# Performance work log

Measured on AMD Instinct MI355X. Metric: run time of the kernel, lower is better.

## Reference

```python
import jax, jax.numpy as jnp
import numpy as np

FACTOR = 3   # ProbAttention factor hardcoded in Informer.__init__
N_HEADS = 8


def _ln(x, g, b, eps=1e-5):
    m = x.mean(-1, keepdims=True)
    v = ((x - m) ** 2).mean(-1, keepdims=True)
    return (x - m) / jnp.sqrt(v + eps) * g + b


def _pos_emb(L, d_model):
    # standard fixed sinusoidal positional embedding (Informer PositionalEmbedding)
    pos = np.arange(L, dtype=np.float32)[:, None]
    div = np.exp(np.arange(0, d_model, 2, dtype=np.float32) * (-np.log(10000.0) / d_model))
    pe = np.zeros((L, d_model), np.float32)
    pe[:, 0::2] = np.sin(pos * div)
    pe[:, 1::2] = np.cos(pos * div)
    return jnp.asarray(pe)


def _prob_attention(q, k, v, rng_key):
    # q,k,v: [B, L, H, D]; mask_flag=False, scale=None -> 1/sqrt(D)
    B, L, H, D = q.shape
    Q = q.transpose(0, 2, 1, 3)
    K = k.transpose(0, 2, 1, 3)
    V = v.transpose(0, 2, 1, 3)
    L_Q = L_K = L
    U_part = min(FACTOR * int(np.ceil(np.log(L_K))), L_K)   # sampled keys per query
    u = min(FACTOR * int(np.ceil(np.log(L_Q))), L_Q)        # top queries kept
    # sample keys (shared across batch/heads, as in torch.randint(L_K,(L_Q,sample_k)))
    idx_sample = jax.random.randint(rng_key, (L_Q, U_part), 0, L_K)
    K_sample = K[:, :, idx_sample, :]                        # [B,H,L_Q,U_part,D]
    QK_sample = jnp.einsum('bhld,bhlsd->bhls', Q, K_sample)  # [B,H,L_Q,U_part]
    M = QK_sample.max(-1) - QK_sample.sum(-1) / L_K          # sparsity measure [B,H,L_Q]
    _, idx_top = jax.lax.top_k(M, u)                         # [B,H,u]
    Q_reduce = jnp.take_along_axis(Q, idx_top[..., None], axis=2)          # [B,H,u,D]
    scores = jnp.einsum('bhud,bhkd->bhuk', Q_reduce, K) / jnp.sqrt(jnp.float32(D))
    attn = jax.nn.softmax(scores, axis=-1)
    upd = jnp.einsum('bhuk,bhkd->bhud', attn, V)             # [B,H,u,D]
    # initial context = mean over values (mask_flag=False), overwrite at top queries
    ctx = jnp.broadcast_to(V.mean(axis=2, keepdims=True), (B, H, L_Q, D))
    bI = jnp.arange(B)[:, None, None]
    hI = jnp.arange(H)[None, :, None]
    ctx = ctx.at[bI, hI, idx_top].set(upd)
    return ctx.transpose(0, 2, 1, 3).reshape(B, L, H * D)


def _forward(x, time_features, g_in, b_in, W_tok, W_time, b_time,
             Wq, bq, Wk, bk, Wv, bv, Wo, bo, W1, b1, W2, b2,
             g1, be1, g2, be2, g_enc, b_enc, W_pre, b_pre, W_fc, b_fc):
    B, L, _ = x.shape
    d_model = W_tok.shape[-1]
    H = N_HEADS
    D = d_model // H
    x = _ln(x, g_in, b_in)                                   # input_norm over enc_in
    # DataEmbedding: circular Conv1d(k=3) token emb + positional + timeF linear
    xp = jnp.pad(x, ((0, 0), (1, 1), (0, 0)), mode='wrap')
    tok = jax.lax.conv_general_dilated(xp, W_tok, (1,), 'VALID',
                                       dimension_numbers=('NWC', 'WIO', 'NWC'))
    h = tok + _pos_emb(L, d_model)[None] + time_features @ W_time.T + b_time
    key = jax.random.key(42)
    for i in range(Wq.shape[0]):                              # e_layers (small, fixed)
        q = (h @ Wq[i].T + bq[i]).reshape(B, L, H, D)
        k = (h @ Wk[i].T + bk[i]).reshape(B, L, H, D)
        v = (h @ Wv[i].T + bv[i]).reshape(B, L, H, D)
        attn_out = _prob_attention(q, k, v, jax.random.fold_in(key, i))
        h = h + attn_out @ Wo[i].T + bo[i]
        h = _ln(h, g1[i], be1[i])
        y = jax.nn.relu(h @ W1[i].T + b1[i]) @ W2[i].T + b2[i]  # 1x1 convs == linears
        h = _ln(h + y, g2[i], be2[i])
    h = _ln(h, g_enc, b_enc)
    last = h[:, -1, :]
    return jax.nn.relu(last @ W_pre.T + b_pre) @ W_fc.T + b_fc


def setup_inputs() -> dict:
    key = jax.random.key(0)
    B, L, C_IN, DM, DFF, E = 8, 2048, 32, 512, 2048, 2
    ks = iter(jax.random.split(key, 48))

    def p(shape, s=0.02):
        return jax.random.normal(next(ks), shape, jnp.float32) * s

    return {
        'x': jax.random.normal(next(ks), (B, L, C_IN), jnp.float32),
        'time_features': jax.random.uniform(next(ks), (B, L, 4), jnp.float32),
        'g_in': jnp.ones((C_IN,), jnp.float32), 'b_in': jnp.zeros((C_IN,), jnp.float32),
        'W_tok': p((3, C_IN, DM)),
        'W_time': p((DM, 4)), 'b_time': jnp.zeros((DM,), jnp.float32),
        'Wq': p((E, DM, DM)), 'bq': jnp.zeros((E, DM), jnp.float32),
        'Wk': p((E, DM, DM)), 'bk': jnp.zeros((E, DM), jnp.float32),
        'Wv': p((E, DM, DM)), 'bv': jnp.zeros((E, DM), jnp.float32),
        'Wo': p((E, DM, DM)), 'bo': jnp.zeros((E, DM), jnp.float32),
        'W1': p((E, DFF, DM)), 'b1': jnp.zeros((E, DFF), jnp.float32),
        'W2': p((E, DM, DFF)), 'b2': jnp.zeros((E, DM), jnp.float32),
        'g1': jnp.ones((E, DM), jnp.float32), 'be1': jnp.zeros((E, DM), jnp.float32),
        'g2': jnp.ones((E, DM), jnp.float32), 'be2': jnp.zeros((E, DM), jnp.float32),
        'g_enc': jnp.ones((DM,), jnp.float32), 'b_enc': jnp.zeros((DM,), jnp.float32),
        'W_pre': p((DM // 2, DM)), 'b_pre': jnp.zeros((DM // 2,), jnp.float32),
        'W_fc': p((1, DM // 2)), 'b_fc': jnp.zeros((1,), jnp.float32),
    }


def reference(x, time_features, g_in, b_in, W_tok, W_time, b_time,
              Wq, bq, Wk, bk, Wv, bv, Wo, bo, W1, b1, W2, b2,
              g1, be1, g2, be2, g_enc, b_enc, W_pre, b_pre, W_fc, b_fc):
    return _forward(x, time_features, g_in, b_in, W_tok, W_time, b_time,
                    Wq, bq, Wk, bk, Wv, bv, Wo, bo, W1, b1, W2, b2,
                    g1, be1, g2, be2, g_enc, b_enc, W_pre, b_pre, W_fc, b_fc)
```

## Files before the change

### kernel.cpp

```cpp
#include <hip/hip_runtime.h>
#include <math.h>

#define BATCH 8
#define SEQ   2048
#define TOK   (BATCH*SEQ)
#define CIN   32
#define DM    512
#define DFF   2048
#define NH    8
#define HD    64
#define NSAMP 24
#define NTOP  24
#define EPS   1e-5f
#define QKVLD 1536

typedef unsigned int u32;
typedef unsigned short u16;
typedef unsigned long long u64;
typedef __attribute__((ext_vector_type(8))) short short8;
typedef __attribute__((ext_vector_type(4))) float floatx4;

__device__ __forceinline__ void async16(const void* g, void* l) {
    __builtin_amdgcn_global_load_lds((const __attribute__((address_space(1))) u32*)g,
                                     (__attribute__((address_space(3))) u32*)l, 16, 0, 0);
}
__device__ __forceinline__ u16 bf16rn(float f) {
    u32 u = __float_as_uint(f);
    return (u16)((u + 0x7fffu + ((u >> 16) & 1u)) >> 16);
}
__device__ __forceinline__ u32 pack_pair(float v) {
    u16 hb = bf16rn(v);
    float r = v - __uint_as_float((u32)hb << 16);
    return (u32)hb | ((u32)bf16rn(r) << 16);
}
__device__ __forceinline__ float unpack_pair(u32 p) {
    return __uint_as_float((p & 0xffffu) << 16) + __uint_as_float(p & 0xffff0000u);
}

__device__ __forceinline__ void tf_round(unsigned &x0, unsigned &x1, int r) {
    x0 += x1;
    x1 = (x1 << r) | (x1 >> (32 - r));
    x1 ^= x0;
}
__device__ __forceinline__ void threefry(unsigned k0, unsigned k1,
                                         unsigned c0, unsigned c1,
                                         unsigned &o0, unsigned &o1) {
    unsigned ks0 = k0, ks1 = k1, ks2 = k0 ^ k1 ^ 0x1BD11BDAu;
    unsigned x0 = c0 + ks0, x1 = c1 + ks1;
    tf_round(x0,x1,13); tf_round(x0,x1,15); tf_round(x0,x1,26); tf_round(x0,x1,6);
    x0 += ks1; x1 += ks2 + 1u;
    tf_round(x0,x1,17); tf_round(x0,x1,29); tf_round(x0,x1,16); tf_round(x0,x1,24);
    x0 += ks2; x1 += ks0 + 2u;
    tf_round(x0,x1,13); tf_round(x0,x1,15); tf_round(x0,x1,26); tf_round(x0,x1,6);
    x0 += ks0; x1 += ks1 + 3u;
    tf_round(x0,x1,17); tf_round(x0,x1,29); tf_round(x0,x1,16); tf_round(x0,x1,24);
    x0 += ks1; x1 += ks2 + 4u;
    tf_round(x0,x1,13); tf_round(x0,x1,15); tf_round(x0,x1,26); tf_round(x0,x1,6);
    x0 += ks2; x1 += ks0 + 5u;
    o0 = x0; o1 = x1;
}

__global__ void sample_kernel(int* __restrict__ idx_sample) {
    const int HALF = (SEQ * NSAMP) / 2;
    int p = blockIdx.x * blockDim.x + threadIdx.x;
    int li = blockIdx.y;
    if (p >= HALF) return;
    unsigned f0, f1;
    threefry(0u, 42u, 0u, (unsigned)li, f0, f1);
    unsigned a0, a1, b0, b1;
    threefry(f0, f1, 0u, 2u, a0, a1);
    threefry(f0, f1, 1u, 3u, b0, b1);
    unsigned o0, o1;
    threefry(a1, b1, (unsigned)p, (unsigned)(p + HALF), o0, o1);
    idx_sample[li * SEQ * NSAMP + p]        = (int)(o0 & (SEQ - 1));
    idx_sample[li * SEQ * NSAMP + p + HALF] = (int)(o1 & (SEQ - 1));
}

__global__ __launch_bounds__(256) void ln_in_kernel(const float* __restrict__ x,
        const float* __restrict__ g, const float* __restrict__ b,
        float* __restrict__ out) {
    int t = blockIdx.x * blockDim.x + threadIdx.x;
    if (t >= TOK) return;
    const float* xr = x + (size_t)t * CIN;
    float vals[CIN];
    float s = 0.f;
#pragma unroll
    for (int c = 0; c < CIN; c++) { vals[c] = xr[c]; s += vals[c]; }
    float m = s * (1.f / CIN);
    float v = 0.f;
#pragma unroll
    for (int c = 0; c < CIN; c++) { float d = vals[c] - m; v += d * d; }
    v *= (1.f / CIN);
    float inv = rsqrtf(v + EPS);
    float* orow = out + (size_t)t * CIN;
#pragma unroll
    for (int c = 0; c < CIN; c++) orow[c] = (vals[c] - m) * inv * g[c] + b[c];
}

__global__ __launch_bounds__(128) void im2col_kernel(const float* __restrict__ xln,
        u32* __restrict__ a) {
    int t = blockIdx.x;
    int j = threadIdx.x;
    if (j >= 96) return;
    int b = t >> 11, l = t & 2047;
    int w = j >> 5, c = j & 31;
    int lw = (l - 1 + w + SEQ) & 2047;
    a[(size_t)t * 96 + j] = pack_pair(xln[(((size_t)b << 11) | lw) * CIN + c]);
}

__global__ __launch_bounds__(256) void wtok_split(const float* __restrict__ Wtok,
        u32* __restrict__ wt) {
    int e = blockIdx.x * 256 + threadIdx.x;
    int o = e / 96, j = e % 96;
    wt[e] = pack_pair(Wtok[(size_t)j * DM + o]);
}

__global__ __launch_bounds__(256) void pe_kernel(float* __restrict__ pe) {
    int e = blockIdx.x * 256 + threadIdx.x;
    int l = e >> 9, o = e & 511;
    const float c1 = -0.017988946039016f;
    int i2 = o & ~1;
    float div = expf((float)i2 * c1);
    float arg = (float)l * div;
    pe[e] = (o & 1) ? cosf(arg) : sinf(arg);
}

__global__ __launch_bounds__(256) void rsd_kernel(const float* __restrict__ pe,
        const float* __restrict__ tfeat, const float* __restrict__ Wtime,
        u32* __restrict__ rsd) {
    int t = blockIdx.x, tid = threadIdx.x;
    int l = t & 2047;
    float t0 = tfeat[(size_t)t * 4], t1 = tfeat[(size_t)t * 4 + 1];
    float t2 = tfeat[(size_t)t * 4 + 2], t3 = tfeat[(size_t)t * 4 + 3];
    for (int o = tid; o < DM; o += 256) {
        float v = pe[l * DM + o]
            + t0 * Wtime[o * 4] + t1 * Wtime[o * 4 + 1]
            + t2 * Wtime[o * 4 + 2] + t3 * Wtime[o * 4 + 3];
        rsd[(size_t)t * DM + o] = pack_pair(v);
    }
}

__global__ __launch_bounds__(256) void split_weights(const float* __restrict__ Wq,
        const float* __restrict__ Wk, const float* __restrict__ Wv,
        const float* __restrict__ Wo, const float* __restrict__ W1,
        const float* __restrict__ W2, u32* __restrict__ out) {
    int i = blockIdx.x * 256 + threadIdx.x;
    const float* src; int off;
    if (i < 1048576) {
        src = (i < 262144) ? Wq : (i < 524288) ? Wk : (i < 786432) ? Wv : Wo;
        off = i & 262143;
    } else if (i < 2097152) { src = W1; off = i - 1048576; }
    else { src = W2; off = i - 2097152; }
    out[i] = pack_pair(src[off]);
}

__global__ void concat_bias(const float* __restrict__ bq, const float* __restrict__ bk,
                            const float* __restrict__ bv, float* __restrict__ o) {
    int i = blockIdx.x * 256 + threadIdx.x;
    o[i] = (i < 512) ? bq[i] : (i < 1024) ? bk[i - 512] : bv[i - 1024];
}

template<bool RELU, bool RESP, bool OUTP>
__global__ __launch_bounds__(256, 2) void gemm_pp(const u32* __restrict__ Ap,
        const u32* __restrict__ Wp, const float* __restrict__ bias,
        const u32* __restrict__ RsdP, float* __restrict__ Cf, u32* __restrict__ Cp,
        int ldc, int K, int lda) {
    __shared__ alignas(16) u32 At[2][4096];
    __shared__ alignas(16) u32 Wt[2][4096];
    const int tid = threadIdx.x;
    int linear = blockIdx.y * gridDim.x + blockIdx.x;
    int xcd = linear & 7, sseq = linear >> 3;
    int mper = gridDim.y >> 3;
    int mt = xcd * mper + (sseq % mper);
    int nt = sseq / mper;
    const int m0 = mt * 128, n0 = nt * 128;
    const int lane = tid & 63, wv = tid >> 6;
    const int wm = wv >> 1, wn = wv & 1;
    const int fr = lane & 15, q = lane >> 4;

    floatx4 acc[4][4] = {};

    const u32* abase = Ap + (size_t)(m0 + (tid >> 1)) * lda + (tid & 1) * 4;
    const u32* wbase = Wp + (size_t)(n0 + (tid >> 1)) * K + (tid & 1) * 4;
    const int doff = tid * 16;
    const int nk = K >> 5;

#pragma unroll
    for (int i = 0; i < 4; i++) {
        async16(abase + i * 8, (char*)At[0] + doff + i * 4096);
        async16(wbase + i * 8, (char*)Wt[0] + doff + i * 4096);
    }

    for (int k = 0; k < nk; k++) {
        const int b = k & 1;
        __syncthreads();
        if (k + 1 < nk) {
            int k0n = (k + 1) << 5;
#pragma unroll
            for (int i = 0; i < 4; i++) {
                async16(abase + k0n + i * 8, (char*)At[b ^ 1] + doff + i * 4096);
                async16(wbase + k0n + i * 8, (char*)Wt[b ^ 1] + doff + i * 4096);
            }
        }
        short8 ah[4], al[4];
#pragma unroll
        for (int mi = 0; mi < 4; mi++) {
            const u32* cell = &At[b][(q * 128 + wm * 64 + mi * 16 + fr) * 8];
            union { u32 u[4]; short8 s; } hh, ll;
            u32 w0 = cell[0], w1 = cell[1], w2 = cell[2], w3 = cell[3];
            u32 w4 = cell[4], w5 = cell[5], w6 = cell[6], w7 = cell[7];
            hh.u[0] = (w0 & 0xffffu) | (w1 << 16);
            hh.u[1] = (w2 & 0xffffu) | (w3 << 16);
            hh.u[2] = (w4 & 0xffffu) | (w5 << 16);
            hh.u[3] = (w6 & 0xffffu) | (w7 << 16);
            ll.u[0] = (w0 >> 16) | (w1 & 0xffff0000u);
            ll.u[1] = (w2 >> 16) | (w3 & 0xffff0000u);
            ll.u[2] = (w4 >> 16) | (w5 & 0xffff0000u);
            ll.u[3] = (w6 >> 16) | (w7 & 0xffff0000u);
            ah[mi] = hh.s; al[mi] = ll.s;
        }
#pragma unroll
        for (int ni = 0; ni < 4; ni++) {
            const u32* cell = &Wt[b][(q * 128 + wn * 64 + ni * 16 + fr) * 8];
            union { u32 u[4]; short8 s; } wh, wl;
            u32 w0 = cell[0], w1 = cell[1], w2 = cell[2], w3 = cell[3];
            u32 w4 = cell[4], w5 = cell[5], w6 = cell[6], w7 = cell[7];
            wh.u[0] = (w0 & 0xffffu) | (w1 << 16);
            wh.u[1] = (w2 & 0xffffu) | (w3 << 16);
            wh.u[2] = (w4 & 0xffffu) | (w5 << 16);
            wh.u[3] = (w6 & 0xffffu) | (w7 << 16);
            wl.u[0] = (w0 >> 16) | (w1 & 0xffff0000u);
            wl.u[1] = (w2 >> 16) | (w3 & 0xffff0000u);
            wl.u[2] = (w4 >> 16) | (w5 & 0xffff0000u);
            wl.u[3] = (w6 >> 16) | (w7 & 0xffff0000u);
#pragma unroll
            for (int mi = 0; mi < 4; mi++) {
                acc[mi][ni] = __builtin_amdgcn_mfma_f32_16x16x32_bf16(ah[mi], wh.s, acc[mi][ni], 0, 0, 0);
                acc[mi][ni] = __builtin_amdgcn_mfma_f32_16x16x32_bf16(ah[mi], wl.s, acc[mi][ni], 0, 0, 0);
                acc[mi][ni] = __builtin_amdgcn_mfma_f32_16x16x32_bf16(al[mi], wh.s, acc[mi][ni], 0, 0, 0);
            }
        }
    }
#pragma unroll
    for (int ni = 0; ni < 4; ni++) {
        int col = n0 + wn * 64 + ni * 16 + fr;
        float bv = bias[col];
#pragma unroll
        for (int mi = 0; mi < 4; mi++) {
            int row = m0 + wm * 64 + mi * 16 + q * 4;
#pragma unroll
            for (int r = 0; r < 4; r++) {
                size_t idx = (size_t)(row + r) * ldc + col;
                float v = acc[mi][ni][r] + bv;
                if (RESP) v += unpack_pair(RsdP[idx]);
                if (RELU) v = fmaxf(v, 0.f);
                if (OUTP) Cp[idx] = pack_pair(v);
                else      Cf[idx] = v;
            }
        }
    }
}

__global__ __launch_bounds__(256) void qk_sample_kernel(const float* __restrict__ qkv,
        const int* __restrict__ idx_sample, float* __restrict__ Mout) {
    int r = (blockIdx.x * 256 + threadIdx.x) >> 6;
    int lane = threadIdx.x & 63;
    if (r >= BATCH * NH * SEQ) return;
    int b = r / (NH * SEQ);
    int head = (r / SEQ) % NH;
    int l = r % SEQ;
    int sidx = lane >> 4, dc = lane & 15;
    const float* qrow = qkv + ((size_t)(b * SEQ + l)) * QKVLD + head * HD + dc * 4;
    float4 qf = *(const float4*)qrow;
    int myidx = (lane < NSAMP) ? idx_sample[l * NSAMP + lane] : 0;
    const float* kbase = qkv + (size_t)b * SEQ * QKVLD + 512 + head * HD + dc * 4;
    int kidx[6];
#pragma unroll
    for (int p = 0; p < 6; p++) kidx[p] = __shfl(myidx, p * 4 + sidx);
    float4 kf[6];
#pragma unroll
    for (int p = 0; p < 6; p++) kf[p] = *(const float4*)(kbase + (size_t)kidx[p] * QKVLD);
    float mx = -INFINITY, sm = 0.f;
#pragma unroll
    for (int p = 0; p < 6; p++) {
        float part = qf.x * kf[p].x + qf.y * kf[p].y + qf.z * kf[p].z + qf.w * kf[p].w;
        part += __shfl_xor(part, 1);
        part += __shfl_xor(part, 2);
        part += __shfl_xor(part, 4);
        part += __shfl_xor(part, 8);
        mx = fmaxf(mx, part);
        sm += part;
    }
    mx = fmaxf(mx, __shfl_xor(mx, 16));
    mx = fmaxf(mx, __shfl_xor(mx, 32));
    sm += __shfl_xor(sm, 16);
    sm += __shfl_xor(sm, 32);
    if (lane == 0) Mout[r] = mx - sm * (1.f / SEQ);
}

__device__ __forceinline__ u64 pack_key(float v, int idx) {
    u32 u = __float_as_uint(v);
    u32 m = (u & 0x80000000u) ? ~u : (u | 0x80000000u);
    return ((u64)m << 32) | (u32)(~(u32)idx);
}

__global__ __launch_bounds__(256) void topk_part(const float* __restrict__ Mbuf,
        u64* __restrict__ cand) {
    __shared__ u64 wred[4];
    int bh = blockIdx.x, chunk = blockIdx.y;
    int tid = threadIdx.x, wv = tid >> 6, lane = tid & 63;
    int l = chunk * 256 + tid;
    u64 val = pack_key(Mbuf[(size_t)bh * SEQ + l], l);
    for (int it = 0; it < NTOP; it++) {
        u64 w = val;
#pragma unroll
        for (int off = 32; off > 0; off >>= 1) {
            u64 o = __shfl_xor(w, off);
            if (o > w) w = o;
        }
        if (lane == 0) wred[wv] = w;
        __syncthreads();
        u64 win = wred[0];
        if (wred[1] > win) win = wred[1];
        if (wred[2] > win) win = wred[2];
        if (wred[3] > win) win = wred[3];
        if (val == win) val = 0;
        if (tid == 0) cand[((size_t)bh * 8 + chunk) * NTOP + it] = win;
        __syncthreads();
    }
}

__global__ __launch_bounds__(256) void topk_merge(const u64* __restrict__ cand,
        int* __restrict__ idx_top) {
    __shared__ u64 wred[4];
    int bh = blockIdx.x;
    int tid = threadIdx.x, wv = tid >> 6, lane = tid & 63;
    u64 val = (tid < 8 * NTOP) ? cand[(size_t)bh * 8 * NTOP + tid] : 0;
    for (int it = 0; it < NTOP; it++) {
        u64 w = val;
#pragma unroll
        for (int off = 32; off > 0; off >>= 1) {
            u64 o = __shfl_xor(w, off);
            if (o > w) w = o;
        }
        if (lane == 0) wred[wv] = w;
        __syncthreads();
        u64 win = wred[0];
        if (wred[1] > win) win = wred[1];
        if (wred[2] > win) win = wred[2];
        if (wred[3] > win) win = wred[3];
        if (val == win) val = 0;
        if (tid == 0) idx_top[bh * NTOP + it] = (int)(~(u32)(win & 0xffffffffull) & (SEQ - 1));
        __syncthreads();
    }
}

__global__ __launch_bounds__(256) void vmean_kernel(const float* __restrict__ qkv,
        float* __restrict__ vmean) {
    __shared__ float red[256];
    int bh = blockIdx.x, slab = blockIdx.y;
    int b = bh >> 3, head = bh & 7;
    int seg = threadIdx.x >> 6, d = threadIdx.x & 63;
    int base_row = slab * 256 + seg * 64;
    float s = 0.f;
    for (int r = 0; r < 64; r++)
        s += qkv[((size_t)(b * SEQ + base_row + r)) * QKVLD + 1024 + head * HD + d];
    red[threadIdx.x] = s;
    __syncthreads();
    if (threadIdx.x < 128) red[threadIdx.x] += red[threadIdx.x + 128];
    __syncthreads();
    if (threadIdx.x < 64) {
        float t = red[threadIdx.x] + red[threadIdx.x + 64];
        atomicAdd(&vmean[bh * HD + d], t * (1.f / SEQ));
    }
}

__global__ void fillctx_kernel(const float* __restrict__ vmean, u32* __restrict__ out) {
    int e = blockIdx.x * 256 + threadIdx.x;
    int c = e & 511;
    int b = e >> 20;
    out[e] = pack_pair(vmean[(((b << 3) | (c >> 6)) << 6) + (c & 63)]);
}

__global__ __launch_bounds__(256) void spattn_flash(const float* __restrict__ qkv,
        const int* __restrict__ idx_top, float* __restrict__ opart,
        float* __restrict__ mspart) {
    __shared__ float KtT[64][65];
    __shared__ float Vt[64][65];
    __shared__ float Qs[24][64];
    __shared__ float Ps[24][66];
    int bh = blockIdx.x, slab = blockIdx.y;
    int b = bh >> 3, h = bh & 7;
    int tid = threadIdx.x;
    int wv = tid >> 6, lane = tid & 63;
    for (int i = tid; i < NTOP * 64; i += 256) {
        int u = i >> 6, d = i & 63;
        int qi = idx_top[bh * NTOP + u];
        Qs[u][d] = qkv[((size_t)(b * SEQ + qi)) * QKVLD + h * HD + d];
    }
    float m[6], s[6], o[6], alpha[6];
#pragma unroll
    for (int j = 0; j < 6; j++) { m[j] = -INFINITY; s[j] = 0.f; o[j] = 0.f; }
    int key0 = slab * 512;
    int sr = tid >> 2, sc0 = (tid & 3) * 16;
    for (int t = 0; t < 8; t++) {
        int kbase = key0 + t * 64;
        __syncthreads();
        const float* kr = qkv + ((size_t)(b * SEQ + kbase + sr)) * QKVLD + 512 + h * HD + sc0;
        const float* vr = qkv + ((size_t)(b * SEQ + kbase + sr)) * QKVLD + 1024 + h * HD + sc0;
        float kf[16], vf[16];
        *(float4*)&kf[0]  = *(const float4*)(kr);
        *(float4*)&kf[4]  = *(const float4*)(kr + 4);
        *(float4*)&kf[8]  = *(const float4*)(kr + 8);
        *(float4*)&kf[12] = *(const float4*)(kr + 12);
        *(float4*)&vf[0]  = *(const float4*)(vr);
        *(float4*)&vf[4]  = *(const float4*)(vr + 4);
        *(float4*)&vf[8]  = *(const float4*)(vr + 8);
        *(float4*)&vf[12] = *(const float4*)(vr + 12);
#pragma unroll
        for (int i = 0; i < 16; i++) {
            KtT[sc0 + i][sr] = kf[i];
            Vt[sr][sc0 + i] = vf[i];
        }
        __syncthreads();
        float dot[6] = {};
#pragma unroll
        for (int d = 0; d < 64; d++) {
            float kv = KtT[d][lane];
#pragma unroll
            for (int j = 0; j < 6; j++) dot[j] += Qs[wv * 6 + j][d] * kv;
        }
#pragma unroll
        for (int j = 0; j < 6; j++) {
            float sc = dot[j] * 0.125f;
            float tmax = sc;
            for (int off = 32; off > 0; off >>= 1) tmax = fmaxf(tmax, __shfl_xor(tmax, off));
            float mn = fmaxf(m[j], tmax);
            float p = __expf(sc - mn);
            float psum = p;
            for (int off = 32; off > 0; off >>= 1) psum += __shfl_xor(psum, off);
            alpha[j] = __expf(m[j] - mn);
            s[j] = s[j] * alpha[j] + psum;
            m[j] = mn;
            Ps[wv * 6 + j][lane] = p;
        }
        float pv[6] = {};
#pragma unroll
        for (int key = 0; key < 64; key++) {
            float vvv = Vt[key][lane];
#pragma unroll
            for (int j = 0; j < 6; j++) pv[j] += Ps[wv * 6 + j][key] * vvv;
        }
#pragma unroll
        for (int j = 0; j < 6; j++) o[j] = o[j] * alpha[j] + pv[j];
    }
    float* ob = opart + ((size_t)(bh * 4 + slab)) * NTOP * 64;
#pragma unroll
    for (int j = 0; j < 6; j++) ob[(wv * 6 + j) * 64 + lane] = o[j];
    if (lane == 0) {
        float* ms = mspart + ((size_t)(bh * 4 + slab)) * NTOP * 2;
#pragma unroll
        for (int j = 0; j < 6; j++) {
            ms[(wv * 6 + j) * 2]     = m[j];
            ms[(wv * 6 + j) * 2 + 1] = s[j];
        }
    }
}

__global__ __launch_bounds__(256) void spattn_combine(const float* __restrict__ opart,
        const float* __restrict__ mspart, const int* __restrict__ idx_top,
        u32* __restrict__ out) {
    __shared__ float wgt[4][NTOP];
    int bh = blockIdx.x;
    int b = bh >> 3, h = bh & 7;
    int tid = threadIdx.x;
    if (tid < NTOP) {
        float mv[4], sv[4];
        float M = -INFINITY;
#pragma unroll
        for (int sl = 0; sl < 4; sl++) {
            mv[sl] = mspart[((size_t)(bh * 4 + sl)) * NTOP * 2 + tid * 2];
            sv[sl] = mspart[((size_t)(bh * 4 + sl)) * NTOP * 2 + tid * 2 + 1];
            M = fmaxf(M, mv[sl]);
        }
        float S = 0.f;
#pragma unroll
        for (int sl = 0; sl < 4; sl++) S += sv[sl] * __expf(mv[sl] - M);
        float invS = 1.f / S;
#pragma unroll
        for (int sl = 0; sl < 4; sl++) wgt[sl][tid] = __expf(mv[sl] - M) * invS;
    }
    __syncthreads();
    for (int i = tid; i < NTOP * 64; i += 256) {
        int u = i >> 6, d = i & 63;
        float val = 0.f;
#pragma unroll
        for (int sl = 0; sl < 4; sl++)
            val += wgt[sl][u] * opart[(((size_t)(bh * 4 + sl)) * NTOP + u) * 64 + d];
        int qi = idx_top[bh * NTOP + u];
        out[((size_t)(b * SEQ + qi)) * DM + h * HD + d] = pack_pair(val);
    }
}

template<bool INP, bool OUTPAIR>
__global__ __launch_bounds__(256) void ln_kernel(const float* __restrict__ srcF,
        const u32* __restrict__ srcP, const float* __restrict__ g,
        const float* __restrict__ b, float* __restrict__ dstF, u32* __restrict__ dstP) {
    int wv = threadIdx.x >> 6, lane = threadIdx.x & 63;
    int t = blockIdx.x * 4 + wv;
    float xv[8];
    if (INP) {
        uint4 p0 = *(const uint4*)&srcP[(size_t)t * DM + lane * 4];
        uint4 p1 = *(const uint4*)&srcP[(size_t)t * DM + lane * 4 + 256];
        xv[0] = unpack_pair(p0.x); xv[1] = unpack_pair(p0.y);
        xv[2] = unpack_pair(p0.z); xv[3] = unpack_pair(p0.w);
        xv[4] = unpack_pair(p1.x); xv[5] = unpack_pair(p1.y);
        xv[6] = unpack_pair(p1.z); xv[7] = unpack_pair(p1.w);
    } else {
        float4 x0 = *(const float4*)&srcF[(size_t)t * DM + lane * 4];
        float4 x1 = *(const float4*)&srcF[(size_t)t * DM + lane * 4 + 256];
        xv[0] = x0.x; xv[1] = x0.y; xv[2] = x0.z; xv[3] = x0.w;
        xv[4] = x1.x; xv[5] = x1.y; xv[6] = x1.z; xv[7] = x1.w;
    }
    float s = 0.f, s2 = 0.f;
#pragma unroll
    for (int i = 0; i < 8; i++) { s += xv[i]; s2 += xv[i] * xv[i]; }
#pragma unroll
    for (int off = 32; off > 0; off >>= 1) {
        s  += __shfl_xor(s, off);
        s2 += __shfl_xor(s2, off);
    }
    float m = s * (1.f / DM);
    float var = s2 * (1.f / DM) - m * m;
    float inv = rsqrtf(var + EPS);
    float4 g0 = *(const float4*)&g[lane * 4];
    float4 g1 = *(const float4*)&g[lane * 4 + 256];
    float4 b0 = *(const float4*)&b[lane * 4];
    float4 b1 = *(const float4*)&b[lane * 4 + 256];
    float y[8];
    y[0] = (xv[0] - m) * inv * g0.x + b0.x;  y[1] = (xv[1] - m) * inv * g0.y + b0.y;
    y[2] = (xv[2] - m) * inv * g0.z + b0.z;  y[3] = (xv[3] - m) * inv * g0.w + b0.w;
    y[4] = (xv[4] - m) * inv * g1.x + b1.x;  y[5] = (xv[5] - m) * inv * g1.y + b1.y;
    y[6] = (xv[6] - m) * inv * g1.z + b1.z;  y[7] = (xv[7] - m) * inv * g1.w + b1.w;
    if (OUTPAIR) {
        uint4 o0, o1;
        o0.x = pack_pair(y[0]); o0.y = pack_pair(y[1]);
        o0.z = pack_pair(y[2]); o0.w = pack_pair(y[3]);
        o1.x = pack_pair(y[4]); o1.y = pack_pair(y[5]);
        o1.z = pack_pair(y[6]); o1.w = pack_pair(y[7]);
        *(uint4*)&dstP[(size_t)t * DM + lane * 4] = o0;
        *(uint4*)&dstP[(size_t)t * DM + lane * 4 + 256] = o1;
    } else {
        float4 o0 = { y[0], y[1], y[2], y[3] };
        float4 o1 = { y[4], y[5], y[6], y[7] };
        *(float4*)&dstF[(size_t)t * DM + lane * 4] = o0;
        *(float4*)&dstF[(size_t)t * DM + lane * 4 + 256] = o1;
    }
}

__global__ __launch_bounds__(256) void head_kernel(const float* __restrict__ hfin,
        const float* __restrict__ Wpre, const float* __restrict__ bpre,
        const float* __restrict__ Wfc, const float* __restrict__ bfc,
        float* __restrict__ out) {
    __shared__ float last[DM];
    __shared__ float red[256];
    int b = blockIdx.x, tid = threadIdx.x;
    const float* hr = hfin + ((size_t)(b * SEQ + SEQ - 1)) * DM;
    last[tid] = hr[tid];
    last[tid + 256] = hr[tid + 256];
    __syncthreads();
    float acc = bpre[tid];
    for (int c = 0; c < DM; c++) acc += last[c] * Wpre[tid * DM + c];
    acc = fmaxf(acc, 0.f);
    red[tid] = acc * Wfc[tid];
    __syncthreads();
    for (int s = 128; s > 0; s >>= 1) { if (tid < s) red[tid] += red[tid + s]; __syncthreads(); }
    if (tid == 0) out[b] = red[0] + bfc[0];
}

extern "C" void kernel_launch(void* const* d_in, const int* in_sizes, int n_in,
                              void* d_out, int out_size, void* d_ws, size_t ws_size,
                              hipStream_t stream) {
    (void)in_sizes; (void)n_in; (void)out_size; (void)ws_size;
    const float* x      = (const float*)d_in[0];
    const float* tfeat  = (const float*)d_in[1];
    const float* g_in   = (const float*)d_in[2];
    const float* b_in   = (const float*)d_in[3];
    const float* W_tok  = (const float*)d_in[4];
    const float* W_time = (const float*)d_in[5];
    const float* b_time = (const float*)d_in[6];
    const float* Wq     = (const float*)d_in[7];
    const float* bq     = (const float*)d_in[8];
    const float* Wk     = (const float*)d_in[9];
    const float* bk     = (const float*)d_in[10];
    const float* Wv     = (const float*)d_in[11];
    const float* bv     = (const float*)d_in[12];
    const float* Wo     = (const float*)d_in[13];
    const float* bo     = (const float*)d_in[14];
    const float* W1     = (const float*)d_in[15];
    const float* b1     = (const float*)d_in[16];
    const float* W2     = (const float*)d_in[17];
    const float* b2     = (const float*)d_in[18];
    const float* g1     = (const float*)d_in[19];
    const float* be1    = (const float*)d_in[20];
    const float* g2     = (const float*)d_in[21];
    const float* be2    = (const float*)d_in[22];
    const float* g_enc  = (const float*)d_in[23];
    const float* b_enc  = (const float*)d_in[24];
    const float* W_pre  = (const float*)d_in[25];
    const float* b_pre  = (const float*)d_in[26];
    const float* W_fc   = (const float*)d_in[27];
    const float* b_fc   = (const float*)d_in[28];
    float* out = (float*)d_out;

    char* ws = (char*)d_ws;
    u32*   hp   = (u32*)(ws);
    float* hf   = (float*)(ws + 33554432);
    char*  bigc = ws + 67108864;
    float* qkv  = (float*)bigc;
    u32*   ctxP = (u32*)(bigc + 100663296);
    u32*   midP = (u32*)bigc;
    float* xln  = (float*)(bigc);
    u32*   acvP = (u32*)(bigc + 2097152);
    float* pe   = (float*)(bigc + 8388608);
    u32*   rsdP = (u32*)(bigc + 12582912);
    u32*   wtok = (u32*)(bigc + 46137344);
    u32*   wpair      = (u32*)(ws + 201326592);
    float* Mbuf       = (float*)(ws + 213909504);
    float* vmean      = (float*)(ws + 214433792);
    int*   idx_sample = (int*)(ws + 214450176);
    int*   idx_top    = (int*)(ws + 214843392);
    float* biasqkv    = (float*)(ws + 214849536);
    u64*   cand       = (u64*)(ws + 214855680);
    float* opart      = (float*)(ws + 214953984);
    float* mspart     = (float*)(ws + 216526848);

    ln_in_kernel<<<TOK / 256, 256, 0, stream>>>(x, g_in, b_in, xln);
    im2col_kernel<<<TOK, 128, 0, stream>>>(xln, acvP);
    wtok_split<<<192, 256, 0, stream>>>(W_tok, wtok);
    pe_kernel<<<4096, 256, 0, stream>>>(pe);
    rsd_kernel<<<TOK, 256, 0, stream>>>(pe, tfeat, W_time, rsdP);
    sample_kernel<<<dim3(96, 2), 256, 0, stream>>>(idx_sample);

    gemm_pp<false, true, true><<<dim3(4, 128), 256, 0, stream>>>(
        acvP, wtok, b_time, rsdP, nullptr, hp, DM, 96, 96);

    const u32* wqkv_p = wpair;
    const u32* wo_p = wpair + 786432;
    const u32* w1_p = wpair + 1048576;
    const u32* w2_p = wpair + 2097152;

    for (int li = 0; li < 2; li++) {
        split_weights<<<12288, 256, 0, stream>>>(
            Wq + (size_t)li * DM * DM, Wk + (size_t)li * DM * DM,
            Wv + (size_t)li * DM * DM, Wo + (size_t)li * DM * DM,
            W1 + (size_t)li * DFF * DM, W2 + (size_t)li * DM * DFF, wpair);
        concat_bias<<<6, 256, 0, stream>>>(bq + (size_t)li * DM, bk + (size_t)li * DM,
                                           bv + (size_t)li * DM, biasqkv);

        const float* bo_i = bo + (size_t)li * DM;
        const float* b1_i = b1 + (size_t)li * DFF;
        const float* b2_i = b2 + (size_t)li * DM;
        const float* g1_i = g1 + (size_t)li * DM;
        const float* be1_i = be1 + (size_t)li * DM;
        const float* g2_i = g2 + (size_t)li * DM;
        const float* be2_i = be2 + (size_t)li * DM;

        gemm_pp<false, false, false><<<dim3(QKVLD / 128, TOK / 128), 256, 0, stream>>>(
            hp, wqkv_p, biasqkv, nullptr, qkv, nullptr, QKVLD, DM, DM);

        qk_sample_kernel<<<(BATCH * NH * SEQ) / 4, 256, 0, stream>>>(
            qkv, idx_sample + li * SEQ * NSAMP, Mbuf);
        topk_part<<<dim3(BATCH * NH, 8), 256, 0, stream>>>(Mbuf, cand);
        topk_merge<<<BATCH * NH, 256, 0, stream>>>(cand, idx_top);
        hipMemsetAsync(vmean, 0, BATCH * NH * HD * sizeof(float), stream);
        vmean_kernel<<<dim3(BATCH * NH, 8), 256, 0, stream>>>(qkv, vmean);
        fillctx_kernel<<<(TOK * DM) / 256, 256, 0, stream>>>(vmean, ctxP);
        spattn_flash<<<dim3(BATCH * NH, 4), 256, 0, stream>>>(qkv, idx_top, opart, mspart);
        spattn_combine<<<BATCH * NH, 256, 0, stream>>>(opart, mspart, idx_top, ctxP);

        gemm_pp<false, true, false><<<dim3(DM / 128, TOK / 128), 256, 0, stream>>>(
            ctxP, wo_p, bo_i, hp, hf, nullptr, DM, DM, DM);
        ln_kernel<false, true><<<TOK / 4, 256, 0, stream>>>(hf, nullptr, g1_i, be1_i, nullptr, hp);

        gemm_pp<true, false, true><<<dim3(DFF / 128, TOK / 128), 256, 0, stream>>>(
            hp, w1_p, b1_i, nullptr, nullptr, midP, DFF, DM, DM);
        gemm_pp<false, true, false><<<dim3(DM / 128, TOK / 128), 256, 0, stream>>>(
            midP, w2_p, b2_i, hp, hf, nullptr, DM, DFF, DFF);
        ln_kernel<false, true><<<TOK / 4, 256, 0, stream>>>(hf, nullptr, g2_i, be2_i, nullptr, hp);
    }

    ln_kernel<true, false><<<TOK / 4, 256, 0, stream>>>(nullptr, hp, g_enc, b_enc, hf, nullptr);
    head_kernel<<<BATCH, 256, 0, stream>>>(hf, W_pre, b_pre, W_fc, b_fc, out);
}
```

Before: 1.306 ms.

## Store split-bf16 operands as separate hi/lo 8-element groups with swizzled LDS

Changes the hi/lo bf16 pair storage from interleaved u32 pairs to a layout where each group of 8 hi values is followed by its 8 lo values. The GEMM can then load MFMA operands straight from LDS as short8 vectors instead of unpacking them with shifts and masks. An XOR swizzle on the global-to-LDS load column aims to avoid bank conflicts. All producers and consumers are rewritten to the new layout (im2col, weight split, residual, LN, fillctx, combine), so any indexing mismatch would corrupt results.

```diff
diff --git a/kernel.cpp b/kernel.cpp
--- a/kernel.cpp
+++ b/kernel.cpp
@@ -18,6 +18,7 @@
 typedef unsigned short u16;
 typedef unsigned long long u64;
 typedef __attribute__((ext_vector_type(8))) short short8;
+typedef __attribute__((ext_vector_type(4))) short short4v;
 typedef __attribute__((ext_vector_type(4))) float floatx4;
 
 __device__ __forceinline__ void async16(const void* g, void* l) {
@@ -28,13 +29,19 @@
     u32 u = __float_as_uint(f);
     return (u16)((u + 0x7fffu + ((u >> 16) & 1u)) >> 16);
 }
-__device__ __forceinline__ u32 pack_pair(float v) {
+__device__ __forceinline__ void sep_store(u16* base, size_t row, int ld2, int j, float v) {
     u16 hb = bf16rn(v);
     float r = v - __uint_as_float((u32)hb << 16);
-    return (u32)hb | ((u32)bf16rn(r) << 16);
-}
-__device__ __forceinline__ float unpack_pair(u32 p) {
-    return __uint_as_float((p & 0xffffu) << 16) + __uint_as_float(p & 0xffff0000u);
+    size_t o = row * (size_t)ld2 + (size_t)((j >> 3) << 4) + (j & 7);
+    base[o] = hb;
+    base[o + 8] = bf16rn(r);
+}
+__device__ __forceinline__ float sep_load(const u16* base, size_t row, int ld2, int j) {
+    size_t o = row * (size_t)ld2 + (size_t)((j >> 3) << 4) + (j & 7);
+    return __uint_as_float((u32)base[o] << 16) + __uint_as_float((u32)base[o + 8] << 16);
+}
+__device__ __forceinline__ float hl2f(u16 h, u16 l) {
+    return __uint_as_float((u32)h << 16) + __uint_as_float((u32)l << 16);
 }
 
 __device__ __forceinline__ void tf_round(unsigned &x0, unsigned &x1, int r) {
@@ -98,21 +105,21 @@
 }
 
 __global__ __launch_bounds__(128) void im2col_kernel(const float* __restrict__ xln,
-        u32* __restrict__ a) {
+        u16* __restrict__ a) {
     int t = blockIdx.x;
     int j = threadIdx.x;
     if (j >= 96) return;
     int b = t >> 11, l = t & 2047;
     int w = j >> 5, c = j & 31;
     int lw = (l - 1 + w + SEQ) & 2047;
-    a[(size_t)t * 96 + j] = pack_pair(xln[(((size_t)b << 11) | lw) * CIN + c]);
+    sep_store(a, (size_t)t, 192, j, xln[(((size_t)b << 11) | lw) * CIN + c]);
 }
 
 __global__ __launch_bounds__(256) void wtok_split(const float* __restrict__ Wtok,
-        u32* __restrict__ wt) {
+        u16* __restrict__ wt) {
     int e = blockIdx.x * 256 + threadIdx.x;
     int o = e / 96, j = e % 96;
-    wt[e] = pack_pair(Wtok[(size_t)j * DM + o]);
+    sep_store(wt, (size_t)o, 192, j, Wtok[(size_t)j * DM + o]);
 }
 
 __global__ __launch_bounds__(256) void pe_kernel(float* __restrict__ pe) {
@@ -127,7 +134,7 @@
 
 __global__ __launch_bounds__(256) void rsd_kernel(const float* __restrict__ pe,
         const float* __restrict__ tfeat, const float* __restrict__ Wtime,
-        u32* __restrict__ rsd) {
+        u16* __restrict__ rsd) {
     int t = blockIdx.x, tid = threadIdx.x;
     int l = t & 2047;
     float t0 = tfeat[(size_t)t * 4], t1 = tfeat[(size_t)t * 4 + 1];
@@ -136,22 +143,27 @@
         float v = pe[l * DM + o]
             + t0 * Wtime[o * 4] + t1 * Wtime[o * 4 + 1]
             + t2 * Wtime[o * 4 + 2] + t3 * Wtime[o * 4 + 3];
-        rsd[(size_t)t * DM + o] = pack_pair(v);
+        sep_store(rsd, (size_t)t, 1024, o, v);
     }
 }
 
 __global__ __launch_bounds__(256) void split_weights(const float* __restrict__ Wq,
         const float* __restrict__ Wk, const float* __restrict__ Wv,
         const float* __restrict__ Wo, const float* __restrict__ W1,
-        const float* __restrict__ W2, u32* __restrict__ out) {
+        const float* __restrict__ W2, u16* __restrict__ out) {
     int i = blockIdx.x * 256 + threadIdx.x;
-    const float* src; int off;
     if (i < 1048576) {
-        src = (i < 262144) ? Wq : (i < 524288) ? Wk : (i < 786432) ? Wv : Wo;
-        off = i & 262143;
-    } else if (i < 2097152) { src = W1; off = i - 1048576; }
-    else { src = W2; off = i - 2097152; }
-    out[i] = pack_pair(src[off]);
+        const float* src = (i < 262144) ? Wq : (i < 524288) ? Wk : (i < 786432) ? Wv : Wo;
+        int off = i & 262143;
+        size_t base = (size_t)(i >> 18) * 524288;
+        sep_store(out + base, (size_t)(off >> 9), 1024, off & 511, src[off]);
+    } else if (i < 2097152) {
+        int off = i - 1048576;
+        sep_store(out + 2097152, (size_t)(off >> 9), 1024, off & 511, W1[off]);
+    } else {
+        int off = i - 2097152;
+        sep_store(out + 4194304, (size_t)(off >> 11), 4096, off & 2047, W2[off]);
+    }
 }
 
 __global__ void concat_bias(const float* __restrict__ bq, const float* __restrict__ bk,
@@ -161,12 +173,12 @@
 }
 
 template<bool RELU, bool RESP, bool OUTP>
-__global__ __launch_bounds__(256, 2) void gemm_pp(const u32* __restrict__ Ap,
-        const u32* __restrict__ Wp, const float* __restrict__ bias,
-        const u32* __restrict__ RsdP, float* __restrict__ Cf, u32* __restrict__ Cp,
+__global__ __launch_bounds__(256, 2) void gemm_pp(const u16* __restrict__ Ap,
+        const u16* __restrict__ Wp, const float* __restrict__ bias,
+        const u16* __restrict__ RsdS, float* __restrict__ Cf, u16* __restrict__ Cp,
         int ldc, int K, int lda) {
-    __shared__ alignas(16) u32 At[2][4096];
-    __shared__ alignas(16) u32 Wt[2][4096];
+    __shared__ alignas(16) u16 At[2][8192];
+    __shared__ alignas(16) u16 Wt[2][8192];
     const int tid = threadIdx.x;
     int linear = blockIdx.y * gridDim.x + blockIdx.x;
     int xcd = linear & 7, sseq = linear >> 3;
@@ -180,64 +192,52 @@
 
     floatx4 acc[4][4] = {};
 
-    const u32* abase = Ap + (size_t)(m0 + (tid >> 1)) * lda + (tid & 1) * 4;
-    const u32* wbase = Wp + (size_t)(n0 + (tid >> 1)) * K + (tid & 1) * 4;
+    const int r0 = tid >> 3;
+    const int gc = (tid & 7) ^ (r0 & 7);
+    const u16* abase = Ap + (size_t)(m0 + r0) * (2 * lda) + gc * 8;
+    const u16* wbase = Wp + (size_t)(n0 + r0) * (2 * K) + gc * 8;
+    const size_t astep = (size_t)32 * 2 * lda;
+    const size_t wstep = (size_t)32 * 2 * K;
     const int doff = tid * 16;
     const int nk = K >> 5;
 
+    const int cph = ((q << 1) ^ (fr & 7)) << 3;
+    const int cpl = ((q << 1) ^ (fr & 7) ^ 1) << 3;
+
 #pragma unroll
     for (int i = 0; i < 4; i++) {
-        async16(abase + i * 8, (char*)At[0] + doff + i * 4096);
-        async16(wbase + i * 8, (char*)Wt[0] + doff + i * 4096);
+        async16(abase + i * astep, (char*)At[0] + doff + i * 4096);
+        async16(wbase + i * wstep, (char*)Wt[0] + doff + i * 4096);
     }
 
     for (int k = 0; k < nk; k++) {
         const int b = k & 1;
         __syncthreads();
         if (k + 1 < nk) {
-            int k0n = (k + 1) << 5;
+            int k2 = (k + 1) << 6;
 #pragma unroll
             for (int i = 0; i < 4; i++) {
-                async16(abase + k0n + i * 8, (char*)At[b ^ 1] + doff + i * 4096);
-                async16(wbase + k0n + i * 8, (char*)Wt[b ^ 1] + doff + i * 4096);
+                async16(abase + k2 + i * astep, (char*)At[b ^ 1] + doff + i * 4096);
+                async16(wbase + k2 + i * wstep, (char*)Wt[b ^ 1] + doff + i * 4096);
             }
         }
         short8 ah[4], al[4];
 #pragma unroll
         for (int mi = 0; mi < 4; mi++) {
-            const u32* cell = &At[b][(q * 128 + wm * 64 + mi * 16 + fr) * 8];
-            union { u32 u[4]; short8 s; } hh, ll;
-            u32 w0 = cell[0], w1 = cell[1], w2 = cell[2], w3 = cell[3];
-            u32 w4 = cell[4], w5 = cell[5], w6 = cell[6], w7 = cell[7];
-            hh.u[0] = (w0 & 0xffffu) | (w1 << 16);
-            hh.u[1] = (w2 & 0xffffu) | (w3 << 16);
-            hh.u[2] = (w4 & 0xffffu) | (w5 << 16);
-            hh.u[3] = (w6 & 0xffffu) | (w7 << 16);
-            ll.u[0] = (w0 >> 16) | (w1 & 0xffff0000u);
-            ll.u[1] = (w2 >> 16) | (w3 & 0xffff0000u);
-            ll.u[2] = (w4 >> 16) | (w5 & 0xffff0000u);
-            ll.u[3] = (w6 >> 16) | (w7 & 0xffff0000u);
-            ah[mi] = hh.s; al[mi] = ll.s;
+            int r = wm * 64 + mi * 16 + fr;
+            ah[mi] = *(const short8*)&At[b][r * 64 + cph];
+            al[mi] = *(const short8*)&At[b][r * 64 + cpl];
         }
 #pragma unroll
         for (int ni = 0; ni < 4; ni++) {
-            const u32* cell = &Wt[b][(q * 128 + wn * 64 + ni * 16 + fr) * 8];
-            union { u32 u[4]; short8 s; } wh, wl;
-            u32 w0 = cell[0], w1 = cell[1], w2 = cell[2], w3 = cell[3];
-            u32 w4 = cell[4], w5 = cell[5], w6 = cell[6], w7 = cell[7];
-            wh.u[0] = (w0 & 0xffffu) | (w1 << 16);
-            wh.u[1] = (w2 & 0xffffu) | (w3 << 16);
-            wh.u[2] = (w4 & 0xffffu) | (w5 << 16);
-            wh.u[3] = (w6 & 0xffffu) | (w7 << 16);
-            wl.u[0] = (w0 >> 16) | (w1 & 0xffff0000u);
-            wl.u[1] = (w2 >> 16) | (w3 & 0xffff0000u);
-            wl.u[2] = (w4 >> 16) | (w5 & 0xffff0000u);
-            wl.u[3] = (w6 >> 16) | (w7 & 0xffff0000u);
+            int r = wn * 64 + ni * 16 + fr;
+            short8 wh8 = *(const short8*)&Wt[b][r * 64 + cph];
+            short8 wl8 = *(const short8*)&Wt[b][r * 64 + cpl];
 #pragma unroll
             for (int mi = 0; mi < 4; mi++) {
-                acc[mi][ni] = __builtin_amdgcn_mfma_f32_16x16x32_bf16(ah[mi], wh.s, acc[mi][ni], 0, 0, 0);
-                acc[mi][ni] = __builtin_amdgcn_mfma_f32_16x16x32_bf16(ah[mi], wl.s, acc[mi][ni], 0, 0, 0);
-                acc[mi][ni] = __builtin_amdgcn_mfma_f32_16x16x32_bf16(al[mi], wh.s, acc[mi][ni], 0, 0, 0);
+                acc[mi][ni] = __builtin_amdgcn_mfma_f32_16x16x32_bf16(ah[mi], wh8, acc[mi][ni], 0, 0, 0);
+                acc[mi][ni] = __builtin_amdgcn_mfma_f32_16x16x32_bf16(ah[mi], wl8, acc[mi][ni], 0, 0, 0);
+                acc[mi][ni] = __builtin_amdgcn_mfma_f32_16x16x32_bf16(al[mi], wh8, acc[mi][ni], 0, 0, 0);
             }
         }
     }
@@ -250,12 +250,11 @@
             int row = m0 + wm * 64 + mi * 16 + q * 4;
 #pragma unroll
             for (int r = 0; r < 4; r++) {
-                size_t idx = (size_t)(row + r) * ldc + col;
                 float v = acc[mi][ni][r] + bv;
-                if (RESP) v += unpack_pair(RsdP[idx]);
+                if (RESP) v += sep_load(RsdS, (size_t)(row + r), 2 * ldc, col);
                 if (RELU) v = fmaxf(v, 0.f);
-                if (OUTP) Cp[idx] = pack_pair(v);
-                else      Cf[idx] = v;
+                if (OUTP) sep_store(Cp, (size_t)(row + r), 2 * ldc, col, v);
+                else      Cf[(size_t)(row + r) * ldc + col] = v;
             }
         }
     }
@@ -375,11 +374,21 @@
     }
 }
 
-__global__ void fillctx_kernel(const float* __restrict__ vmean, u32* __restrict__ out) {
+__global__ void fillctx_kernel(const float* __restrict__ vmean, u16* __restrict__ out) {
     int e = blockIdx.x * 256 + threadIdx.x;
-    int c = e & 511;
-    int b = e >> 20;
-    out[e] = pack_pair(vmean[(((b << 3) | (c >> 6)) << 6) + (c & 63)]);
+    int t = e >> 6, g = e & 63;
+    const float* vm = vmean + ((((t >> 11) << 3) | (g >> 3)) << 6) + (g & 7) * 8;
+    short8 hh, ll;
+#pragma unroll
+    for (int s = 0; s < 8; s++) {
+        float v = vm[s];
+        u16 hb = bf16rn(v);
+        hh[s] = (short)hb;
+        ll[s] = (short)bf16rn(v - __uint_as_float((u32)hb << 16));
+    }
+    u16* dp = out + (size_t)t * 1024 + g * 16;
+    *(short8*)dp = hh;
+    *(short8*)(dp + 8) = ll;
 }
 
 __global__ __launch_bounds__(256) void spattn_flash(const float* __restrict__ qkv,
@@ -469,7 +478,7 @@
 
 __global__ __launch_bounds__(256) void spattn_combine(const float* __restrict__ opart,
         const float* __restrict__ mspart, const int* __restrict__ idx_top,
-        u32* __restrict__ out) {
+        u16* __restrict__ out) {
     __shared__ float wgt[4][NTOP];
     int bh = blockIdx.x;
     int b = bh >> 3, h = bh & 7;
@@ -498,24 +507,28 @@
         for (int sl = 0; sl < 4; sl++)
             val += wgt[sl][u] * opart[(((size_t)(bh * 4 + sl)) * NTOP + u) * 64 + d];
         int qi = idx_top[bh * NTOP + u];
-        out[((size_t)(b * SEQ + qi)) * DM + h * HD + d] = pack_pair(val);
-    }
-}
-
-template<bool INP, bool OUTPAIR>
+        sep_store(out, (size_t)(b * SEQ + qi), 1024, h * HD + d, val);
+    }
+}
+
+template<bool INP, bool OUTSEP>
 __global__ __launch_bounds__(256) void ln_kernel(const float* __restrict__ srcF,
-        const u32* __restrict__ srcP, const float* __restrict__ g,
-        const float* __restrict__ b, float* __restrict__ dstF, u32* __restrict__ dstP) {
+        const u16* __restrict__ srcS, const float* __restrict__ g,
+        const float* __restrict__ b, float* __restrict__ dstF, u16* __restrict__ dstS) {
     int wv = threadIdx.x >> 6, lane = threadIdx.x & 63;
     int t = blockIdx.x * 4 + wv;
     float xv[8];
     if (INP) {
-        uint4 p0 = *(const uint4*)&srcP[(size_t)t * DM + lane * 4];
-        uint4 p1 = *(const uint4*)&srcP[(size_t)t * DM + lane * 4 + 256];
-        xv[0] = unpack_pair(p0.x); xv[1] = unpack_pair(p0.y);
-        xv[2] = unpack_pair(p0.z); xv[3] = unpack_pair(p0.w);
-        xv[4] = unpack_pair(p1.x); xv[5] = unpack_pair(p1.y);
-        xv[6] = unpack_pair(p1.z); xv[7] = unpack_pair(p1.w);
+        const u16* sp = srcS + (size_t)t * 1024 + (lane >> 1) * 16 + (lane & 1) * 4;
+        short4v h0 = *(const short4v*)sp;
+        short4v l0 = *(const short4v*)(sp + 8);
+        short4v h1 = *(const short4v*)(sp + 512);
+        short4v l1 = *(const short4v*)(sp + 520);
+#pragma unroll
+        for (int i = 0; i < 4; i++) {
+            xv[i]     = hl2f((u16)h0[i], (u16)l0[i]);
+            xv[i + 4] = hl2f((u16)h1[i], (u16)l1[i]);
+        }
     } else {
         float4 x0 = *(const float4*)&srcF[(size_t)t * DM + lane * 4];
         float4 x1 = *(const float4*)&srcF[(size_t)t * DM + lane * 4 + 256];
@@ -542,14 +555,22 @@
     y[2] = (xv[2] - m) * inv * g0.z + b0.z;  y[3] = (xv[3] - m) * inv * g0.w + b0.w;
     y[4] = (xv[4] - m) * inv * g1.x + b1.x;  y[5] = (xv[5] - m) * inv * g1.y + b1.y;
     y[6] = (xv[6] - m) * inv * g1.z + b1.z;  y[7] = (xv[7] - m) * inv * g1.w + b1.w;
-    if (OUTPAIR) {
-        uint4 o0, o1;
-        o0.x = pack_pair(y[0]); o0.y = pack_pair(y[1]);
-        o0.z = pack_pair(y[2]); o0.w = pack_pair(y[3]);
-        o1.x = pack_pair(y[4]); o1.y = pack_pair(y[5]);
-        o1.z = pack_pair(y[6]); o1.w = pack_pair(y[7]);
-        *(uint4*)&dstP[(size_t)t * DM + lane * 4] = o0;
-        *(uint4*)&dstP[(size_t)t * DM + lane * 4 + 256] = o1;
+    if (OUTSEP) {
+        u16* dp = dstS + (size_t)t * 1024 + (lane >> 1) * 16 + (lane & 1) * 4;
+        short4v hh0, ll0, hh1, ll1;
+#pragma unroll
+        for (int i = 0; i < 4; i++) {
+            u16 hb = bf16rn(y[i]);
+            hh0[i] = (short)hb;
+            ll0[i] = (short)bf16rn(y[i] - __uint_as_float((u32)hb << 16));
+            u16 hb2 = bf16rn(y[i + 4]);
+            hh1[i] = (short)hb2;
+            ll1[i] = (short)bf16rn(y[i + 4] - __uint_as_float((u32)hb2 << 16));
+        }
+        *(short4v*)dp = hh0;
+        *(short4v*)(dp + 8) = ll0;
+        *(short4v*)(dp + 512) = hh1;
+        *(short4v*)(dp + 520) = ll1;
     } else {
         float4 o0 = { y[0], y[1], y[2], y[3] };
         float4 o1 = { y[4], y[5], y[6], y[7] };
@@ -614,18 +635,18 @@
     float* out = (float*)d_out;
 
     char* ws = (char*)d_ws;
-    u32*   hp   = (u32*)(ws);
+    u16*   hp   = (u16*)(ws);
     float* hf   = (float*)(ws + 33554432);
     char*  bigc = ws + 67108864;
     float* qkv  = (float*)bigc;
-    u32*   ctxP = (u32*)(bigc + 100663296);
-    u32*   midP = (u32*)bigc;
+    u16*   ctxP = (u16*)(bigc + 100663296);
+    u16*   midP = (u16*)bigc;
     float* xln  = (float*)(bigc);
-    u32*   acvP = (u32*)(bigc + 2097152);
+    u16*   acvP = (u16*)(bigc + 2097152);
     float* pe   = (float*)(bigc + 8388608);
-    u32*   rsdP = (u32*)(bigc + 12582912);
-    u32*   wtok = (u32*)(bigc + 46137344);
-    u32*   wpair      = (u32*)(ws + 201326592);
+    u16*   rsdS = (u16*)(bigc + 12582912);
+    u16*   wtok = (u16*)(bigc + 46137344);
+    u16*   wsep       = (u16*)(ws + 201326592);
     float* Mbuf       = (float*)(ws + 213909504);
     float* vmean      = (float*)(ws + 214433792);
     int*   idx_sample = (int*)(ws + 214450176);
@@ -639,22 +660,22 @@
     im2col_kernel<<<TOK, 128, 0, stream>>>(xln, acvP);
     wtok_split<<<192, 256, 0, stream>>>(W_tok, wtok);
     pe_kernel<<<4096, 256, 0, stream>>>(pe);
-    rsd_kernel<<<TOK, 256, 0, stream>>>(pe, tfeat, W_time, rsdP);
+    rsd_kernel<<<TOK, 256, 0, stream>>>(pe, tfeat, W_time, rsdS);
     sample_kernel<<<dim3(96, 2), 256, 0, stream>>>(idx_sample);
 
     gemm_pp<false, true, true><<<dim3(4, 128), 256, 0, stream>>>(
-        acvP, wtok, b_time, rsdP, nullptr, hp, DM, 96, 96);
-
-    const u32* wqkv_p = wpair;
-    const u32* wo_p = wpair + 786432;
-    const u32* w1_p = wpair + 1048576;
-    const u32* w2_p = wpair + 2097152;
+        acvP, wtok, b_time, rsdS, nullptr, hp, DM, 96, 96);
+
+    const u16* wqkv_p = wsep;
+    const u16* wo_p = wsep + 1572864;
+    const u16* w1_p = wsep + 2097152;
+    const u16* w2_p = wsep + 4194304;
 
     for (int li = 0; li < 2; li++) {
         split_weights<<<12288, 256, 0, stream>>>(
             Wq + (size_t)li * DM * DM, Wk + (size_t)li * DM * DM,
             Wv + (size_t)li * DM * DM, Wo + (size_t)li * DM * DM,
-            W1 + (size_t)li * DFF * DM, W2 + (size_t)li * DM * DFF, wpair);
+            W1 + (size_t)li * DFF * DM, W2 + (size_t)li * DM * DFF, wsep);
         concat_bias<<<6, 256, 0, stream>>>(bq + (size_t)li * DM, bk + (size_t)li * DM,
                                            bv + (size_t)li * DM, biasqkv);
 
@@ -675,7 +696,7 @@
         topk_merge<<<BATCH * NH, 256, 0, stream>>>(cand, idx_top);
         hipMemsetAsync(vmean, 0, BATCH * NH * HD * sizeof(float), stream);
         vmean_kernel<<<dim3(BATCH * NH, 8), 256, 0, stream>>>(qkv, vmean);
-        fillctx_kernel<<<(TOK * DM) / 256, 256, 0, stream>>>(vmean, ctxP);
+        fillctx_kernel<<<(TOK * 64) / 256, 256, 0, stream>>>(vmean, ctxP);
         spattn_flash<<<dim3(BATCH * NH, 4), 256, 0, stream>>>(qkv, idx_top, opart, mspart);
         spattn_combine<<<BATCH * NH, 256, 0, stream>>>(opart, mspart, idx_top, ctxP);
 
```

After: 1.190 ms. -8.9%, faster.
